# Kernel tuning notes

Hardware: AMD Instinct MI355X
Metric: run time of the kernel (lower is better)

The kernel has to match this reference:

```python
import jax, jax.numpy as jnp
import numpy as np

N = 2_000_000   # total instances (sum of bag sizes Nk)
C = 128         # number of classes
M = 100_000     # number of bags


def setup_inputs() -> dict:
    key = jax.random.key(0)
    k1, k2 = jax.random.split(key)
    input_ = jax.random.normal(k1, (N, C), dtype=jnp.float32)
    target = jax.random.randint(k2, (M,), 0, C, dtype=jnp.int32)
    # Contiguous bag ids 0..M-1, every bag nonempty (avg ~20 instances/bag),
    # sorted as the torch loop implicitly assumes grouped/contiguous bags.
    bag = jnp.sort(jnp.arange(N, dtype=jnp.int32) % M)
    return {"input_": input_, "target": target, "bag": bag}


def reference(input_, target, bag):
    # Per-bag max over instance logits: [N, C] -> [M, C]
    bag_logits = jax.ops.segment_max(input_, bag, num_segments=M)
    # Cross entropy with mean reduction (F.cross_entropy default)
    logz = jax.scipy.special.logsumexp(bag_logits, axis=1)          # [M]
    picked = jnp.take_along_axis(bag_logits, target[:, None], axis=1)[:, 0]
    return jnp.mean(logz - picked)
```

## Files before the change

### kernel.cpp

```cpp
#include <hip/hip_runtime.h>
#include <math.h>

#define CLS 128

__global__ __launch_bounds__(256) void find_starts_kernel(
    const int* __restrict__ bag, int* __restrict__ starts, int N, int M) {
    int i = blockIdx.x * blockDim.x + threadIdx.x;
    if (i >= N) return;
    if (i == 0) {
        starts[bag[0]] = 0;
        starts[M] = N;
    } else if (bag[i] != bag[i - 1]) {
        starts[bag[i]] = i;
    }
}

__global__ __launch_bounds__(CLS) void bag_loss_kernel(
    const float* __restrict__ input, const int* __restrict__ target,
    const int* __restrict__ starts, float* __restrict__ losses) {
    const int m = blockIdx.x;
    const int c = threadIdx.x;
    const int s = starts[m];
    const int e = starts[m + 1];

    float mx = -INFINITY;
    const float* p = input + (size_t)s * CLS + c;
    for (int i = s; i < e; ++i, p += CLS) {
        mx = fmaxf(mx, *p);
    }

    __shared__ float vals[CLS];
    __shared__ float red[CLS];
    vals[c] = mx;
    red[c] = mx;
    __syncthreads();

    #pragma unroll
    for (int off = CLS / 2; off > 0; off >>= 1) {
        if (c < off) red[c] = fmaxf(red[c], red[c + off]);
        __syncthreads();
    }
    const float bigmax = red[0];
    __syncthreads();

    red[c] = expf(vals[c] - bigmax);
    __syncthreads();
    #pragma unroll
    for (int off = CLS / 2; off > 0; off >>= 1) {
        if (c < off) red[c] += red[c + off];
        __syncthreads();
    }

    if (c == 0) {
        const float logz = bigmax + logf(red[0]);
        losses[m] = logz - vals[target[m]];
    }
}

__global__ __launch_bounds__(256) void reduce_partial_kernel(
    const float* __restrict__ losses, float* __restrict__ partials, int M) {
    __shared__ float sm[256];
    float s = 0.f;
    for (int i = blockIdx.x * 256 + threadIdx.x; i < M; i += gridDim.x * 256)
        s += losses[i];
    sm[threadIdx.x] = s;
    __syncthreads();
    #pragma unroll
    for (int off = 128; off > 0; off >>= 1) {
        if (threadIdx.x < off) sm[threadIdx.x] += sm[threadIdx.x + off];
        __syncthreads();
    }
    if (threadIdx.x == 0) partials[blockIdx.x] = sm[0];
}

__global__ __launch_bounds__(256) void reduce_final_kernel(
    const float* __restrict__ partials, float* __restrict__ out, float invM) {
    __shared__ float sm[256];
    sm[threadIdx.x] = partials[threadIdx.x];
    __syncthreads();
    #pragma unroll
    for (int off = 128; off > 0; off >>= 1) {
        if (threadIdx.x < off) sm[threadIdx.x] += sm[threadIdx.x + off];
        __syncthreads();
    }
    if (threadIdx.x == 0) out[0] = sm[0] * invM;
}

extern "C" void kernel_launch(void* const* d_in, const int* in_sizes, int n_in,
                              void* d_out, int out_size, void* d_ws, size_t ws_size,
                              hipStream_t stream) {
    const float* input  = (const float*)d_in[0];
    const int*   target = (const int*)d_in[1];
    const int*   bag    = (const int*)d_in[2];
    const int M = in_sizes[1];
    const int N = in_sizes[2];
    float* out = (float*)d_out;

    char* ws = (char*)d_ws;
    int* starts = (int*)ws;
    size_t off = ((size_t)(M + 1) * sizeof(int) + 255) & ~(size_t)255;
    float* losses = (float*)(ws + off);
    off += ((size_t)M * sizeof(float) + 255) & ~(size_t)255;
    float* partials = (float*)(ws + off);

    find_starts_kernel<<<(N + 255) / 256, 256, 0, stream>>>(bag, starts, N, M);
    bag_loss_kernel<<<M, CLS, 0, stream>>>(input, target, starts, losses);
    reduce_partial_kernel<<<256, 256, 0, stream>>>(losses, partials, M);
    reduce_final_kernel<<<1, 256, 0, stream>>>(partials, out, 1.0f / M);
}
```

Before: 1.373 ms.

## Vectorize bag max with float4 loads and use wavefront shuffle reductions

The per-bag max now reads the bag's rows as a flat float4 stream, with 128 threads each covering four classes and two independent accumulators, instead of one scalar strided load per class per row. The shared-memory tree reductions with many __syncthreads are replaced by a single shared fold to 32 lanes, followed by xor-shuffle reductions for the max and the exp-sum and a shuffle to fetch the target logit. This is meant to raise memory-level parallelism and cut synchronisation overhead in what is a bandwidth-bound pass. It relies on the float4 lane mapping (index mod 32) lining up with class groups, which holds because the stride of 128 float4s is a multiple of 32.

```diff
diff --git a/kernel.cpp b/kernel.cpp
--- a/kernel.cpp
+++ b/kernel.cpp
@@ -2,6 +2,14 @@
 #include <math.h>
 
 #define CLS 128
+
+__device__ __forceinline__ float4 fmax4(float4 a, float4 b) {
+    a.x = fmaxf(a.x, b.x);
+    a.y = fmaxf(a.y, b.y);
+    a.z = fmaxf(a.z, b.z);
+    a.w = fmaxf(a.w, b.w);
+    return a;
+}
 
 __global__ __launch_bounds__(256) void find_starts_kernel(
     const int* __restrict__ bag, int* __restrict__ starts, int N, int M) {
@@ -19,41 +27,52 @@
     const float* __restrict__ input, const int* __restrict__ target,
     const int* __restrict__ starts, float* __restrict__ losses) {
     const int m = blockIdx.x;
-    const int c = threadIdx.x;
+    const int t = threadIdx.x;
     const int s = starts[m];
     const int e = starts[m + 1];
 
-    float mx = -INFINITY;
-    const float* p = input + (size_t)s * CLS + c;
-    for (int i = s; i < e; ++i, p += CLS) {
-        mx = fmaxf(mx, *p);
+    const float4* __restrict__ base = (const float4*)(input + (size_t)s * CLS);
+    const int nf4 = (e - s) * (CLS / 4);
+
+    float4 a0 = make_float4(-INFINITY, -INFINITY, -INFINITY, -INFINITY);
+    float4 a1 = a0;
+    for (int k = t; k < nf4; k += 256) {
+        float4 v = base[k];
+        const int k2 = k + 128;
+        if (k2 < nf4) {
+            float4 w = base[k2];
+            a1 = fmax4(a1, w);
+        }
+        a0 = fmax4(a0, v);
     }
+    a0 = fmax4(a0, a1);
 
-    __shared__ float vals[CLS];
-    __shared__ float red[CLS];
-    vals[c] = mx;
-    red[c] = mx;
+    __shared__ float4 sm[CLS];
+    sm[t] = a0;
     __syncthreads();
 
-    #pragma unroll
-    for (int off = CLS / 2; off > 0; off >>= 1) {
-        if (c < off) red[c] = fmaxf(red[c], red[c + off]);
-        __syncthreads();
-    }
-    const float bigmax = red[0];
-    __syncthreads();
+    if (t < 32) {
+        const float4 f = fmax4(fmax4(sm[t], sm[t + 32]),
+                               fmax4(sm[t + 64], sm[t + 96]));
 
-    red[c] = expf(vals[c] - bigmax);
-    __syncthreads();
-    #pragma unroll
-    for (int off = CLS / 2; off > 0; off >>= 1) {
-        if (c < off) red[c] += red[c + off];
-        __syncthreads();
-    }
+        float lm = fmaxf(fmaxf(f.x, f.y), fmaxf(f.z, f.w));
+        #pragma unroll
+        for (int mask = 16; mask > 0; mask >>= 1)
+            lm = fmaxf(lm, __shfl_xor(lm, mask, 64));
 
-    if (c == 0) {
-        const float logz = bigmax + logf(red[0]);
-        losses[m] = logz - vals[target[m]];
+        float ssum = expf(f.x - lm) + expf(f.y - lm) +
+                     expf(f.z - lm) + expf(f.w - lm);
+        #pragma unroll
+        for (int mask = 16; mask > 0; mask >>= 1)
+            ssum += __shfl_xor(ssum, mask, 64);
+
+        const int tc = target[m];
+        const int src = tc >> 2;
+        const int elem = tc & 3;
+        float pf = (elem == 0) ? f.x : (elem == 1) ? f.y : (elem == 2) ? f.z : f.w;
+        const float picked = __shfl(pf, src, 64);
+
+        if (t == 0) losses[m] = lm + logf(ssum) - picked;
     }
 }
 
```

New measurement: 1.260 ms. 8.2% less time.
